# Kernel tuning notes

Hardware: AMD Instinct MI355X
Metric: run time of the kernel (lower is better)

The kernel has to match this reference:

```python
import jax, jax.numpy as jnp
import numpy as np
import math

B, L, H, E = 4, 1024, 8, 64  # win_size = L
NEG_INF = -1e9  # finite stand-in for -inf causal mask (same softmax result, grad-safe)


def setup_inputs() -> dict:
    key = jax.random.key(0)
    k1, k2, k3, k4 = jax.random.split(key, 4)
    return {
        "queries": jax.random.normal(k1, (B, L, H, E), dtype=jnp.float32),
        "keys": jax.random.normal(k2, (B, L, H, E), dtype=jnp.float32),
        "values": jax.random.normal(k3, (B, L, H, E), dtype=jnp.float32),
        "sigma": jax.random.normal(k4, (B, L, H), dtype=jnp.float32),
    }


def reference(queries, keys, values, sigma):
    b, l, h, e = queries.shape
    scale = 1.0 / math.sqrt(e)

    # attention scores: [B,H,L,S]
    scores = jnp.einsum('blhe,bshe->bhls', queries, keys)
    causal = jnp.triu(jnp.ones((l, l), dtype=bool), k=1)  # mask_flag=True, attn_mask=None
    scores = jnp.where(causal, NEG_INF, scores)
    attn = scale * scores

    # sigma chain: [B,L,H] -> [B,H,L] -> [B,H,L,L]
    s = jnp.transpose(sigma, (0, 2, 1))
    s = jax.nn.sigmoid(s * 5.0) + 1e-5
    s = jnp.power(3.0, s) - 1.0
    sigma4 = jnp.broadcast_to(s[..., None], (b, h, l, l))

    # gaussian prior over |i-j| distances
    idx = jnp.arange(l)
    dist = jnp.abs(idx[:, None] - idx[None, :]).astype(attn.dtype)  # [L,L]
    prior = jnp.exp(-(dist ** 2) / (2.0 * sigma4 ** 2)) / (math.sqrt(2.0 * math.pi) * sigma4)

    series = jax.nn.softmax(attn, axis=-1)  # dropout is identity at eval
    V = jnp.einsum('bhls,bshd->blhd', series, values)
    return V, series, prior, sigma4
```

## Files before the change

kernel.cpp:

```cpp
#include <hip/hip_runtime.h>
#include <math.h>
#include <stdint.h>


#define BB 4
#define LL 1024
#define HH 8
#define EE 64
#define ROWS 32
#define THREADS 1024
#define CHUNK 128
#define VCHUNK 64

typedef __attribute__((ext_vector_type(8))) short bf16x8;
typedef __attribute__((ext_vector_type(4))) float f32x4;

static constexpr size_t OFF_V      = 0;
static constexpr size_t OFF_SERIES = (size_t)BB * LL * HH * EE;
static constexpr size_t OFF_PRIOR  = OFF_SERIES + (size_t)BB * HH * LL * LL;
static constexpr size_t OFF_SIGMA4 = OFF_PRIOR + (size_t)BB * HH * LL * LL;

static constexpr int LDS_BYTES = 81920;

__device__ __forceinline__ short f2bf(float f) {
    union { float f; uint32_t u; } v; v.f = f;
    uint32_t r = (v.u + 0x7FFFu + ((v.u >> 16) & 1u)) >> 16;
    return (short)r;
}
__device__ __forceinline__ float bf2f(short s) {
    union { uint32_t u; float f; } v; v.u = ((uint32_t)(unsigned short)s) << 16;
    return v.f;
}

__global__ __launch_bounds__(THREADS, 8) void anomaly_attn_kernel(
    const float* __restrict__ Q, const float* __restrict__ K,
    const float* __restrict__ V, float* __restrict__ out)
{
    extern __shared__ char lds[];
    short* sSb  = (short*)lds;
    short* Kb   = (short*)(lds + 65536);
    short* Vt   = (short*)(lds + 65536);
    float* red  = (float*)(lds + 73728);
    float* rinv = (float*)(lds + 77824);

    const int tid  = threadIdx.x;
    const int lane = tid & 63;
    const int w    = tid >> 6;
    const int tile = blockIdx.x & 31;
    const int bh   = blockIdx.x >> 5;
    const int b    = bh >> 3, h = bh & 7;
    const int r0   = tile * ROWS;
    const int NCH  = (r0 + ROWS + CHUNK - 1) / CHUNK;
    const int NC   = NCH * CHUNK;

    const float* Kbase = K + (size_t)b * (LL * HH * EE) + h * EE;
    const float* Vbase = V + (size_t)b * (LL * HH * EE) + h * EE;

    const int jr2 = tid >> 3;
    const int g8  = tid & 7;

    const int rgQ = w >> 3;
    const int cgQ = w & 7;
    bf16x8 qf0, qf1;
    {
        int qrow = r0 + rgQ * 16 + (lane & 15);
        const float* qp = Q + ((size_t)(b * LL + qrow) * HH + h) * EE + ((lane >> 4) << 3);
        float4 a = *(const float4*)qp;
        float4 c = *(const float4*)(qp + 4);
        qf0[0]=f2bf(a.x); qf0[1]=f2bf(a.y); qf0[2]=f2bf(a.z); qf0[3]=f2bf(a.w);
        qf0[4]=f2bf(c.x); qf0[5]=f2bf(c.y); qf0[6]=f2bf(c.z); qf0[7]=f2bf(c.w);
        float4 a2 = *(const float4*)(qp + 32);
        float4 c2 = *(const float4*)(qp + 36);
        qf1[0]=f2bf(a2.x); qf1[1]=f2bf(a2.y); qf1[2]=f2bf(a2.z); qf1[3]=f2bf(a2.w);
        qf1[4]=f2bf(c2.x); qf1[5]=f2bf(c2.y); qf1[6]=f2bf(c2.z); qf1[7]=f2bf(c2.w);
    }

    float4 kp0 = *(const float4*)&Kbase[(size_t)jr2 * 512 + g8 * 8];
    float4 kp1 = *(const float4*)&Kbase[(size_t)jr2 * 512 + g8 * 8 + 4];

    for (int ck = 0; ck < NCH; ++ck) {
        __syncthreads();
        {
            bf16x8 kv;
            kv[0]=f2bf(kp0.x); kv[1]=f2bf(kp0.y); kv[2]=f2bf(kp0.z); kv[3]=f2bf(kp0.w);
            kv[4]=f2bf(kp1.x); kv[5]=f2bf(kp1.y); kv[6]=f2bf(kp1.z); kv[7]=f2bf(kp1.w);
            *(bf16x8*)&Kb[jr2 * 64 + ((g8 ^ (jr2 & 7)) << 3)] = kv;
        }
        if (ck + 1 < NCH) {
            kp0 = *(const float4*)&Kbase[(size_t)((ck + 1) * CHUNK + jr2) * 512 + g8 * 8];
            kp1 = *(const float4*)&Kbase[(size_t)((ck + 1) * CHUNK + jr2) * 512 + g8 * 8 + 4];
        }
        __syncthreads();

        f32x4 acc = {0.f, 0.f, 0.f, 0.f};
        const int jl = cgQ * 16 + (lane & 15);
        {
            int ge = lane >> 4;
            bf16x8 bf = *(const bf16x8*)&Kb[jl * 64 + ((ge ^ (jl & 7)) << 3)];
            acc = __builtin_amdgcn_mfma_f32_16x16x32_bf16(qf0, bf, acc, 0, 0, 0);
            ge = 4 + (lane >> 4);
            bf16x8 bf2 = *(const bf16x8*)&Kb[jl * 64 + ((ge ^ (jl & 7)) << 3)];
            acc = __builtin_amdgcn_mfma_f32_16x16x32_bf16(qf1, bf2, acc, 0, 0, 0);
        }
        int colg = ck * CHUNK + cgQ * 16 + (lane & 15);
        int gc   = colg >> 3;
        int co   = colg & 7;
#pragma unroll
        for (int q = 0; q < 4; ++q) {
            int rt = rgQ * 16 + ((lane >> 4) << 2) + q;
            float e = (colg <= r0 + rt) ? __expf(acc[q] * 0.125f) : 0.f;
            sSb[rt * 1024 + ((gc ^ (rt & 7)) << 3) + co] = f2bf(e);
        }
    }
    __syncthreads();

    const int vj = tid >> 4;
    const int ve = (tid & 15) * 4;
    float4 vp = *(const float4*)&Vbase[(size_t)vj * 512 + ve];

    {
        int r = tid >> 5, j2 = tid & 31;
        float sum = 0.f;
        for (int g = j2; g < (NC >> 3); g += 32) {
            bf16x8 v = *(const bf16x8*)&sSb[r * 1024 + ((g ^ (r & 7)) << 3)];
            float s0 = bf2f(v[0]) + bf2f(v[1]), s1 = bf2f(v[2]) + bf2f(v[3]);
            float s2 = bf2f(v[4]) + bf2f(v[5]), s3 = bf2f(v[6]) + bf2f(v[7]);
            sum += (s0 + s1) + (s2 + s3);
        }
        sum += __shfl_xor(sum, 1);
        sum += __shfl_xor(sum, 2);
        sum += __shfl_xor(sum, 4);
        sum += __shfl_xor(sum, 8);
        sum += __shfl_xor(sum, 16);
        if (j2 == 0) rinv[r] = 1.0f / sum;
    }
    __syncthreads();

    {
        int gc = tid & 127;
        int rb = tid >> 7;
        size_t base = OFF_SERIES + ((size_t)bh * LL + r0) * LL;
#pragma unroll
        for (int it = 0; it < 4; ++it) {
            int r_ = rb + it * 8;
            float4 o0, o1;
            if (gc * 8 < NC) {
                float ri = rinv[r_];
                bf16x8 v = *(const bf16x8*)&sSb[r_ * 1024 + ((gc ^ (r_ & 7)) << 3)];
                o0 = make_float4(bf2f(v[0]) * ri, bf2f(v[1]) * ri, bf2f(v[2]) * ri, bf2f(v[3]) * ri);
                o1 = make_float4(bf2f(v[4]) * ri, bf2f(v[5]) * ri, bf2f(v[6]) * ri, bf2f(v[7]) * ri);
            } else {
                o0 = make_float4(0.f, 0.f, 0.f, 0.f); o1 = o0;
            }
            *(float4*)(out + base + (size_t)r_ * LL + gc * 8)     = o0;
            *(float4*)(out + base + (size_t)r_ * LL + gc * 8 + 4) = o1;
        }
    }

    const int t   = w & 7;
    const int rgP = t >> 2;
    const int egP = t & 3;
    const int kh  = w >> 3;
    const int NVC = NC / VCHUNK;
    f32x4 pacc = {0.f, 0.f, 0.f, 0.f};

    for (int vc = 0; vc < NVC; ++vc) {
        __syncthreads();
        {
            float vv[4] = {vp.x, vp.y, vp.z, vp.w};
            int jg = vj >> 3, jo = vj & 7;
#pragma unroll
            for (int i = 0; i < 4; ++i) {
                int e = ve + i;
                Vt[e * 64 + ((jg ^ (e & 7)) << 3) + jo] = f2bf(vv[i]);
            }
        }
        if (vc + 1 < NVC) {
            vp = *(const float4*)&Vbase[(size_t)((vc + 1) * VCHUNK + vj) * 512 + ve];
        }
        __syncthreads();

        {
            int rt = rgP * 16 + (lane & 15);
            int gg = vc * 8 + kh * 4 + (lane >> 4);
            bf16x8 af = *(const bf16x8*)&sSb[rt * 1024 + ((gg ^ (rt & 7)) << 3)];
            int e  = egP * 16 + (lane & 15);
            int g  = kh * 4 + (lane >> 4);
            bf16x8 bf = *(const bf16x8*)&Vt[e * 64 + ((g ^ (e & 7)) << 3)];
            pacc = __builtin_amdgcn_mfma_f32_16x16x32_bf16(af, bf, pacc, 0, 0, 0);
        }
    }

    __syncthreads();
    if (kh == 0 && t < 4) *(f32x4*)&red[(t * 64 + lane) * 4] = pacc;
    __syncthreads();
    if (kh == 1 && t < 4) {
        f32x4 o = *(const f32x4*)&red[(t * 64 + lane) * 4];
#pragma unroll
        for (int q = 0; q < 4; ++q) {
            int rt = rgP * 16 + ((lane >> 4) << 2) + q;
            out[OFF_V + ((size_t)(b * LL + r0 + rt) * HH + h) * EE + egP * 16 + (lane & 15)]
                = (pacc[q] + o[q]) * rinv[rt];
        }
    }
    __syncthreads();
    if (kh == 0 && t >= 4) *(f32x4*)&red[((t - 4) * 64 + lane) * 4] = pacc;
    __syncthreads();
    if (kh == 1 && t >= 4) {
        f32x4 o = *(const f32x4*)&red[((t - 4) * 64 + lane) * 4];
#pragma unroll
        for (int q = 0; q < 4; ++q) {
            int rt = rgP * 16 + ((lane >> 4) << 2) + q;
            out[OFF_V + ((size_t)(b * LL + r0 + rt) * HH + h) * EE + egP * 16 + (lane & 15)]
                = (pacc[q] + o[q]) * rinv[rt];
        }
    }
}

__global__ __launch_bounds__(256) void anomaly_prior_kernel(
    const float* __restrict__ sigma, float* __restrict__ out)
{
    int bhrow = blockIdx.x;
    int i  = bhrow & (LL - 1);
    int bh = bhrow >> 10;
    int b  = bh >> 3, h = bh & 7;

    float x  = sigma[((size_t)b * LL + i) * HH + h];
    float sg = 1.0f / (1.0f + __expf(-5.0f * x)) + 1e-5f;
    float s  = __expf(1.0986122886681098f * sg) - 1.0f;
    float inv2s2 = 0.5f / (s * s);
    float coef   = 0.3989422804014327f / s;

    size_t rowbase = (size_t)bhrow * LL;
    int j0 = threadIdx.x * 4;

    float d0 = (float)(i - (j0 + 0));
    float d1 = (float)(i - (j0 + 1));
    float d2 = (float)(i - (j0 + 2));
    float d3 = (float)(i - (j0 + 3));
    float4 p = make_float4(coef * __expf(-d0 * d0 * inv2s2),
                           coef * __expf(-d1 * d1 * inv2s2),
                           coef * __expf(-d2 * d2 * inv2s2),
                           coef * __expf(-d3 * d3 * inv2s2));
    *(float4*)(out + OFF_PRIOR + rowbase + j0)  = p;
    *(float4*)(out + OFF_SIGMA4 + rowbase + j0) = make_float4(s, s, s, s);
}

extern "C" void kernel_launch(void* const* d_in, const int* in_sizes, int n_in,
                              void* d_out, int out_size, void* d_ws, size_t ws_size,
                              hipStream_t stream) {
    const float* Q     = (const float*)d_in[0];
    const float* K     = (const float*)d_in[1];
    const float* V     = (const float*)d_in[2];
    const float* sigma = (const float*)d_in[3];
    float* out = (float*)d_out;

    (void)hipFuncSetAttribute((const void*)anomaly_attn_kernel,
                              hipFuncAttributeMaxDynamicSharedMemorySize, LDS_BYTES);

    anomaly_attn_kernel<<<dim3(BB * HH * (LL / ROWS)), dim3(THREADS), LDS_BYTES, stream>>>(Q, K, V, out);
    anomaly_prior_kernel<<<dim3(BB * HH * LL), dim3(256), 0, stream>>>(sigma, out);
}
```

Before: 474.0 us.

## Fuse prior/sigma output into attention kernel and shrink tiles to 16 rows

Merges the separate prior/sigma4 kernel into the attention kernel, so each block also writes the prior and sigma4 rows for its query rows. Tile size drops from 32 to 16 rows with 512 threads. K is now loaded straight from global into registers per wave and fed to MFMA without LDS staging or per-chunk barriers. This removes a kernel launch and the K-chunk synchronisation and raises block count and occupancy, at the cost of reading K and V more often and adding prior-writing work to each block.

Measured after the change: 488.9 us. 1.03x slower.

```diff
diff --git a/kernel.cpp b/kernel.cpp
--- a/kernel.cpp
+++ b/kernel.cpp
@@ -7,10 +7,8 @@
 #define LL 1024
 #define HH 8
 #define EE 64
-#define ROWS 32
-#define THREADS 1024
-#define CHUNK 128
-#define VCHUNK 64
+#define ROWS 16
+#define THREADS 512
 
 typedef __attribute__((ext_vector_type(8))) short bf16x8;
 typedef __attribute__((ext_vector_type(4))) float f32x4;
@@ -20,7 +18,7 @@
 static constexpr size_t OFF_PRIOR  = OFF_SERIES + (size_t)BB * HH * LL * LL;
 static constexpr size_t OFF_SIGMA4 = OFF_PRIOR + (size_t)BB * HH * LL * LL;
 
-static constexpr int LDS_BYTES = 81920;
+static constexpr int LDS_BYTES = 45184;
 
 __device__ __forceinline__ short f2bf(float f) {
     union { float f; uint32_t u; } v; v.f = f;
@@ -32,38 +30,42 @@
     return v.f;
 }
 
-__global__ __launch_bounds__(THREADS, 8) void anomaly_attn_kernel(
+__global__ __launch_bounds__(THREADS, 6) void anomaly_fused_kernel(
     const float* __restrict__ Q, const float* __restrict__ K,
-    const float* __restrict__ V, float* __restrict__ out)
+    const float* __restrict__ V, const float* __restrict__ sigma,
+    float* __restrict__ out)
 {
     extern __shared__ char lds[];
-    short* sSb  = (short*)lds;
-    short* Kb   = (short*)(lds + 65536);
-    short* Vt   = (short*)(lds + 65536);
-    float* red  = (float*)(lds + 73728);
-    float* rinv = (float*)(lds + 77824);
+    short* sS   = (short*)lds;
+    short* Vt   = (short*)(lds + 32768);
+    float* red  = (float*)(lds + 40960);
+    float* rinv = (float*)(lds + 45056);
+    float* ssig = (float*)(lds + 45120);
 
     const int tid  = threadIdx.x;
     const int lane = tid & 63;
     const int w    = tid >> 6;
-    const int tile = blockIdx.x & 31;
-    const int bh   = blockIdx.x >> 5;
+    const int tile = blockIdx.x & 63;
+    const int bh   = blockIdx.x >> 6;
     const int b    = bh >> 3, h = bh & 7;
     const int r0   = tile * ROWS;
-    const int NCH  = (r0 + ROWS + CHUNK - 1) / CHUNK;
-    const int NC   = NCH * CHUNK;
+    const int ntiles = (r0 >> 4) + 1;
+    const int NC     = r0 + 16;
+    const int NCpad  = (NC + 63) & ~63;
+    const int NVC    = NCpad >> 6;
 
     const float* Kbase = K + (size_t)b * (LL * HH * EE) + h * EE;
     const float* Vbase = V + (size_t)b * (LL * HH * EE) + h * EE;
 
-    const int jr2 = tid >> 3;
-    const int g8  = tid & 7;
-
-    const int rgQ = w >> 3;
-    const int cgQ = w & 7;
+    for (int x = tid; x < (NCpad - NC) * ROWS; x += THREADS) {
+        int r_ = x & 15;
+        int c  = NC + (x >> 4);
+        sS[r_ * 1024 + (((c >> 3) ^ (r_ & 7)) << 3) + (c & 7)] = 0;
+    }
+
     bf16x8 qf0, qf1;
     {
-        int qrow = r0 + rgQ * 16 + (lane & 15);
+        int qrow = r0 + (lane & 15);
         const float* qp = Q + ((size_t)(b * LL + qrow) * HH + h) * EE + ((lane >> 4) << 3);
         float4 a = *(const float4*)qp;
         float4 c = *(const float4*)(qp + 4);
@@ -75,54 +77,53 @@
         qf1[4]=f2bf(c2.x); qf1[5]=f2bf(c2.y); qf1[6]=f2bf(c2.z); qf1[7]=f2bf(c2.w);
     }
 
-    float4 kp0 = *(const float4*)&Kbase[(size_t)jr2 * 512 + g8 * 8];
-    float4 kp1 = *(const float4*)&Kbase[(size_t)jr2 * 512 + g8 * 8 + 4];
-
-    for (int ck = 0; ck < NCH; ++ck) {
-        __syncthreads();
-        {
-            bf16x8 kv;
-            kv[0]=f2bf(kp0.x); kv[1]=f2bf(kp0.y); kv[2]=f2bf(kp0.z); kv[3]=f2bf(kp0.w);
-            kv[4]=f2bf(kp1.x); kv[5]=f2bf(kp1.y); kv[6]=f2bf(kp1.z); kv[7]=f2bf(kp1.w);
-            *(bf16x8*)&Kb[jr2 * 64 + ((g8 ^ (jr2 & 7)) << 3)] = kv;
-        }
-        if (ck + 1 < NCH) {
-            kp0 = *(const float4*)&Kbase[(size_t)((ck + 1) * CHUNK + jr2) * 512 + g8 * 8];
-            kp1 = *(const float4*)&Kbase[(size_t)((ck + 1) * CHUNK + jr2) * 512 + g8 * 8 + 4];
-        }
-        __syncthreads();
-
-        f32x4 acc = {0.f, 0.f, 0.f, 0.f};
-        const int jl = cgQ * 16 + (lane & 15);
-        {
-            int ge = lane >> 4;
-            bf16x8 bf = *(const bf16x8*)&Kb[jl * 64 + ((ge ^ (jl & 7)) << 3)];
-            acc = __builtin_amdgcn_mfma_f32_16x16x32_bf16(qf0, bf, acc, 0, 0, 0);
-            ge = 4 + (lane >> 4);
-            bf16x8 bf2 = *(const bf16x8*)&Kb[jl * 64 + ((ge ^ (jl & 7)) << 3)];
-            acc = __builtin_amdgcn_mfma_f32_16x16x32_bf16(qf1, bf2, acc, 0, 0, 0);
-        }
-        int colg = ck * CHUNK + cgQ * 16 + (lane & 15);
-        int gc   = colg >> 3;
-        int co   = colg & 7;
-#pragma unroll
-        for (int q = 0; q < 4; ++q) {
-            int rt = rgQ * 16 + ((lane >> 4) << 2) + q;
-            float e = (colg <= r0 + rt) ? __expf(acc[q] * 0.125f) : 0.f;
-            sSb[rt * 1024 + ((gc ^ (rt & 7)) << 3) + co] = f2bf(e);
-        }
-    }
-    __syncthreads();
-
-    const int vj = tid >> 4;
-    const int ve = (tid & 15) * 4;
-    float4 vp = *(const float4*)&Vbase[(size_t)vj * 512 + ve];
+    {
+        const int jro = lane & 15;
+        const int eo  = (lane >> 4) << 3;
+        float4 ka, kb, kc, kd;
+        int jt = w;
+        if (jt < ntiles) {
+            const float* kp = Kbase + (size_t)(jt * 16 + jro) * 512 + eo;
+            ka = *(const float4*)kp;       kb = *(const float4*)(kp + 4);
+            kc = *(const float4*)(kp + 32); kd = *(const float4*)(kp + 36);
+        }
+        for (; jt < ntiles; jt += 8) {
+            float4 c0 = ka, c1 = kb, c2 = kc, c3 = kd;
+            if (jt + 8 < ntiles) {
+                const float* kp = Kbase + (size_t)((jt + 8) * 16 + jro) * 512 + eo;
+                ka = *(const float4*)kp;       kb = *(const float4*)(kp + 4);
+                kc = *(const float4*)(kp + 32); kd = *(const float4*)(kp + 36);
+            }
+            bf16x8 b0, b1;
+            b0[0]=f2bf(c0.x); b0[1]=f2bf(c0.y); b0[2]=f2bf(c0.z); b0[3]=f2bf(c0.w);
+            b0[4]=f2bf(c1.x); b0[5]=f2bf(c1.y); b0[6]=f2bf(c1.z); b0[7]=f2bf(c1.w);
+            b1[0]=f2bf(c2.x); b1[1]=f2bf(c2.y); b1[2]=f2bf(c2.z); b1[3]=f2bf(c2.w);
+            b1[4]=f2bf(c3.x); b1[5]=f2bf(c3.y); b1[6]=f2bf(c3.z); b1[7]=f2bf(c3.w);
+            f32x4 acc = {0.f, 0.f, 0.f, 0.f};
+            acc = __builtin_amdgcn_mfma_f32_16x16x32_bf16(qf0, b0, acc, 0, 0, 0);
+            acc = __builtin_amdgcn_mfma_f32_16x16x32_bf16(qf1, b1, acc, 0, 0, 0);
+            int col = jt * 16 + jro;
+            int gc = col >> 3, co = col & 7;
+#pragma unroll
+            for (int q = 0; q < 4; ++q) {
+                int rt = ((lane >> 4) << 2) + q;
+                float e = (col <= r0 + rt) ? __expf(acc[q] * 0.125f) : 0.f;
+                sS[rt * 1024 + ((gc ^ (rt & 7)) << 3) + co] = f2bf(e);
+            }
+        }
+    }
+    __syncthreads();
+
+    const int vj  = tid >> 3;
+    const int ve8 = (tid & 7) * 8;
+    float4 vp0 = *(const float4*)&Vbase[(size_t)vj * 512 + ve8];
+    float4 vp1 = *(const float4*)&Vbase[(size_t)vj * 512 + ve8 + 4];
 
     {
         int r = tid >> 5, j2 = tid & 31;
         float sum = 0.f;
-        for (int g = j2; g < (NC >> 3); g += 32) {
-            bf16x8 v = *(const bf16x8*)&sSb[r * 1024 + ((g ^ (r & 7)) << 3)];
+        for (int g = j2; g < (NCpad >> 3); g += 32) {
+            bf16x8 v = *(const bf16x8*)&sS[r * 1024 + ((g ^ (r & 7)) << 3)];
             float s0 = bf2f(v[0]) + bf2f(v[1]), s1 = bf2f(v[2]) + bf2f(v[3]);
             float s2 = bf2f(v[4]) + bf2f(v[5]), s3 = bf2f(v[6]) + bf2f(v[7]);
             sum += (s0 + s1) + (s2 + s3);
@@ -133,117 +134,109 @@
         sum += __shfl_xor(sum, 8);
         sum += __shfl_xor(sum, 16);
         if (j2 == 0) rinv[r] = 1.0f / sum;
-    }
-    __syncthreads();
-
-    {
-        int gc = tid & 127;
-        int rb = tid >> 7;
+        if (j2 == 1) {
+            float x  = sigma[((size_t)b * LL + r0 + r) * HH + h];
+            float sg = 1.0f / (1.0f + __expf(-5.0f * x)) + 1e-5f;
+            ssig[r]  = __expf(1.0986122886681098f * sg) - 1.0f;
+        }
+    }
+    __syncthreads();
+
+    const int gc128 = tid & 127;
+    const int rb    = tid >> 7;
+
+    {
         size_t base = OFF_SERIES + ((size_t)bh * LL + r0) * LL;
 #pragma unroll
         for (int it = 0; it < 4; ++it) {
-            int r_ = rb + it * 8;
+            int r_ = rb + it * 4;
             float4 o0, o1;
-            if (gc * 8 < NC) {
+            if (gc128 * 8 < NC) {
                 float ri = rinv[r_];
-                bf16x8 v = *(const bf16x8*)&sSb[r_ * 1024 + ((gc ^ (r_ & 7)) << 3)];
-                o0 = make_float4(bf2f(v[0]) * ri, bf2f(v[1]) * ri, bf2f(v[2]) * ri, bf2f(v[3]) * ri);
-                o1 = make_float4(bf2f(v[4]) * ri, bf2f(v[5]) * ri, bf2f(v[6]) * ri, bf2f(v[7]) * ri);
+                bf16x8 v = *(const bf16x8*)&sS[r_ * 1024 + ((gc128 ^ (r_ & 7)) << 3)];
+                o0 = make_float4(bf2f(v[0])*ri, bf2f(v[1])*ri, bf2f(v[2])*ri, bf2f(v[3])*ri);
+                o1 = make_float4(bf2f(v[4])*ri, bf2f(v[5])*ri, bf2f(v[6])*ri, bf2f(v[7])*ri);
             } else {
                 o0 = make_float4(0.f, 0.f, 0.f, 0.f); o1 = o0;
             }
-            *(float4*)(out + base + (size_t)r_ * LL + gc * 8)     = o0;
-            *(float4*)(out + base + (size_t)r_ * LL + gc * 8 + 4) = o1;
-        }
-    }
-
-    const int t   = w & 7;
-    const int rgP = t >> 2;
-    const int egP = t & 3;
-    const int kh  = w >> 3;
-    const int NVC = NC / VCHUNK;
+            *(float4*)(out + base + (size_t)r_ * LL + gc128 * 8)     = o0;
+            *(float4*)(out + base + (size_t)r_ * LL + gc128 * 8 + 4) = o1;
+        }
+    }
+
+    {
+        size_t pbase = (size_t)bh * LL + r0;
+#pragma unroll
+        for (int it = 0; it < 4; ++it) {
+            int r_ = rb + it * 4;
+            int i  = r0 + r_;
+            float s      = ssig[r_];
+            float inv2s2 = 0.5f / (s * s);
+            float coef   = 0.3989422804014327f / s;
+            int j0 = gc128 * 8;
+            float4 p0, p1;
+            {
+                float d0 = (float)(i - (j0 + 0)), d1 = (float)(i - (j0 + 1));
+                float d2 = (float)(i - (j0 + 2)), d3 = (float)(i - (j0 + 3));
+                p0 = make_float4(coef * __expf(-d0*d0*inv2s2), coef * __expf(-d1*d1*inv2s2),
+                                 coef * __expf(-d2*d2*inv2s2), coef * __expf(-d3*d3*inv2s2));
+                float d4 = (float)(i - (j0 + 4)), d5 = (float)(i - (j0 + 5));
+                float d6 = (float)(i - (j0 + 6)), d7 = (float)(i - (j0 + 7));
+                p1 = make_float4(coef * __expf(-d4*d4*inv2s2), coef * __expf(-d5*d5*inv2s2),
+                                 coef * __expf(-d6*d6*inv2s2), coef * __expf(-d7*d7*inv2s2));
+            }
+            size_t rowb = (pbase + r_) * LL + j0;
+            *(float4*)(out + OFF_PRIOR + rowb)      = p0;
+            *(float4*)(out + OFF_PRIOR + rowb + 4)  = p1;
+            *(float4*)(out + OFF_SIGMA4 + rowb)     = make_float4(s, s, s, s);
+            *(float4*)(out + OFF_SIGMA4 + rowb + 4) = make_float4(s, s, s, s);
+        }
+    }
+
+    const int eg = w & 3;
+    const int kh = w >> 2;
     f32x4 pacc = {0.f, 0.f, 0.f, 0.f};
 
     for (int vc = 0; vc < NVC; ++vc) {
         __syncthreads();
         {
-            float vv[4] = {vp.x, vp.y, vp.z, vp.w};
+            float vv[8] = {vp0.x, vp0.y, vp0.z, vp0.w, vp1.x, vp1.y, vp1.z, vp1.w};
             int jg = vj >> 3, jo = vj & 7;
 #pragma unroll
-            for (int i = 0; i < 4; ++i) {
-                int e = ve + i;
+            for (int i = 0; i < 8; ++i) {
+                int e = ve8 + i;
                 Vt[e * 64 + ((jg ^ (e & 7)) << 3) + jo] = f2bf(vv[i]);
             }
         }
         if (vc + 1 < NVC) {
-            vp = *(const float4*)&Vbase[(size_t)((vc + 1) * VCHUNK + vj) * 512 + ve];
+            vp0 = *(const float4*)&Vbase[(size_t)((vc + 1) * 64 + vj) * 512 + ve8];
+            vp1 = *(const float4*)&Vbase[(size_t)((vc + 1) * 64 + vj) * 512 + ve8 + 4];
         }
         __syncthreads();
 
         {
-            int rt = rgP * 16 + (lane & 15);
+            int rt = lane & 15;
             int gg = vc * 8 + kh * 4 + (lane >> 4);
-            bf16x8 af = *(const bf16x8*)&sSb[rt * 1024 + ((gg ^ (rt & 7)) << 3)];
-            int e  = egP * 16 + (lane & 15);
-            int g  = kh * 4 + (lane >> 4);
-            bf16x8 bf = *(const bf16x8*)&Vt[e * 64 + ((g ^ (e & 7)) << 3)];
+            bf16x8 af = *(const bf16x8*)&sS[rt * 1024 + ((gg ^ (rt & 7)) << 3)];
+            int e  = eg * 16 + (lane & 15);
+            int jg = kh * 4 + (lane >> 4);
+            bf16x8 bf = *(const bf16x8*)&Vt[e * 64 + ((jg ^ (e & 7)) << 3)];
             pacc = __builtin_amdgcn_mfma_f32_16x16x32_bf16(af, bf, pacc, 0, 0, 0);
         }
     }
 
     __syncthreads();
-    if (kh == 0 && t < 4) *(f32x4*)&red[(t * 64 + lane) * 4] = pacc;
-    __syncthreads();
-    if (kh == 1 && t < 4) {
-        f32x4 o = *(const f32x4*)&red[(t * 64 + lane) * 4];
+    if (kh == 0) *(f32x4*)&red[(eg * 64 + lane) * 4] = pacc;
+    __syncthreads();
+    if (kh == 1) {
+        f32x4 o = *(const f32x4*)&red[(eg * 64 + lane) * 4];
 #pragma unroll
         for (int q = 0; q < 4; ++q) {
-            int rt = rgP * 16 + ((lane >> 4) << 2) + q;
-            out[OFF_V + ((size_t)(b * LL + r0 + rt) * HH + h) * EE + egP * 16 + (lane & 15)]
+            int rt = ((lane >> 4) << 2) + q;
+            out[OFF_V + ((size_t)(b * LL + r0 + rt) * HH + h) * EE + eg * 16 + (lane & 15)]
                 = (pacc[q] + o[q]) * rinv[rt];
         }
     }
-    __syncthreads();
-    if (kh == 0 && t >= 4) *(f32x4*)&red[((t - 4) * 64 + lane) * 4] = pacc;
-    __syncthreads();
-    if (kh == 1 && t >= 4) {
-        f32x4 o = *(const f32x4*)&red[((t - 4) * 64 + lane) * 4];
-#pragma unroll
-        for (int q = 0; q < 4; ++q) {
-            int rt = rgP * 16 + ((lane >> 4) << 2) + q;
-            out[OFF_V + ((size_t)(b * LL + r0 + rt) * HH + h) * EE + egP * 16 + (lane & 15)]
-                = (pacc[q] + o[q]) * rinv[rt];
-        }
-    }
-}
-
-__global__ __launch_bounds__(256) void anomaly_prior_kernel(
-    const float* __restrict__ sigma, float* __restrict__ out)
-{
-    int bhrow = blockIdx.x;
-    int i  = bhrow & (LL - 1);
-    int bh = bhrow >> 10;
-    int b  = bh >> 3, h = bh & 7;
-
-    float x  = sigma[((size_t)b * LL + i) * HH + h];
-    float sg = 1.0f / (1.0f + __expf(-5.0f * x)) + 1e-5f;
-    float s  = __expf(1.0986122886681098f * sg) - 1.0f;
-    float inv2s2 = 0.5f / (s * s);
-    float coef   = 0.3989422804014327f / s;
-
-    size_t rowbase = (size_t)bhrow * LL;
-    int j0 = threadIdx.x * 4;
-
-    float d0 = (float)(i - (j0 + 0));
-    float d1 = (float)(i - (j0 + 1));
-    float d2 = (float)(i - (j0 + 2));
-    float d3 = (float)(i - (j0 + 3));
-    float4 p = make_float4(coef * __expf(-d0 * d0 * inv2s2),
-                           coef * __expf(-d1 * d1 * inv2s2),
-                           coef * __expf(-d2 * d2 * inv2s2),
-                           coef * __expf(-d3 * d3 * inv2s2));
-    *(float4*)(out + OFF_PRIOR + rowbase + j0)  = p;
-    *(float4*)(out + OFF_SIGMA4 + rowbase + j0) = make_float4(s, s, s, s);
 }
 
 extern "C" void kernel_launch(void* const* d_in, const int* in_sizes, int n_in,
@@ -255,9 +248,6 @@
     const float* sigma = (const float*)d_in[3];
     float* out = (float*)d_out;
 
-    (void)hipFuncSetAttribute((const void*)anomaly_attn_kernel,
-                              hipFuncAttributeMaxDynamicSharedMemorySize, LDS_BYTES);
-
-    anomaly_attn_kernel<<<dim3(BB * HH * (LL / ROWS)), dim3(THREADS), LDS_BYTES, stream>>>(Q, K, V, out);
-    anomaly_prior_kernel<<<dim3(BB * HH * LL), dim3(256), 0, stream>>>(sigma, out);
-}
+    anomaly_fused_kernel<<<dim3(BB * HH * (LL / ROWS)), dim3(THREADS), LDS_BYTES, stream>>>(
+        Q, K, V, sigma, out);
+}
```
